# Kernel tuning notes

Measured on AMD Instinct MI355X. Metric: run time of the kernel, lower is better.

The kernel has to match this reference:

```python
import jax, jax.numpy as jnp
import numpy as np
import math

N = 4096      # n_history
D = 512       # embed_dim
H = 8         # time-weight MLP hidden size


def setup_inputs() -> dict:
    key = jax.random.key(0)
    k1, k2, k3, k4, k5 = jax.random.split(key, 5)
    return {
        "query_code_embeds": jax.random.normal(k1, (N, D), dtype=jnp.float32),
        "hist_embeddings": jax.random.normal(k2, (N, D), dtype=jnp.float32),
        "hist_times": jax.random.uniform(k3, (N,), dtype=jnp.float32),
        "tw_w1": jax.random.normal(k4, (1, H), dtype=jnp.float32) * (1.0 / math.sqrt(1.0)),
        "tw_b1": jnp.zeros((H,), dtype=jnp.float32),
        "tw_w2": jax.random.normal(k5, (H, 1), dtype=jnp.float32) * (1.0 / math.sqrt(H)),
        "tw_b2": jnp.zeros((1,), dtype=jnp.float32),
    }


def reference(query_code_embeds, hist_embeddings, hist_times, tw_w1, tw_b1, tw_w2, tw_b2):
    # pairwise absolute time differences: [n, n, 1]
    time_diffs = jnp.abs(hist_times[:, None] - hist_times[None, :])[..., None]
    # pointwise MLP on time diffs -> multiplicative attention bias [n, n]
    h = jax.nn.relu(time_diffs @ tw_w1 + tw_b1)            # [n, n, H]
    time_weights = jax.nn.sigmoid(h @ tw_w2 + tw_b2)[..., 0]  # [n, n]
    # scaled dot-product scores modulated by time weights
    scores = (query_code_embeds @ hist_embeddings.T) / math.sqrt(D)
    scores = scores * time_weights
    attn = jax.nn.softmax(scores, axis=1)
    return attn @ hist_embeddings
```

## Files before the change

kernel.cpp:

```cpp
#include <hip/hip_runtime.h>

#define N 4096
#define D 512
#define FRAG_SH 512
#define NTHR 256
#define SC_STRIDE 136
#define SMEM_BYTES 69632
#define BUF_SH 12288

typedef __attribute__((ext_vector_type(8))) short short8;
typedef __attribute__((ext_vector_type(4))) float f32x4;
typedef const __attribute__((address_space(1))) unsigned int* gptr_t;
typedef __attribute__((address_space(3))) unsigned int* lptr_t;

__device__ __forceinline__ unsigned short f2bf(float f) {
    unsigned int u = __float_as_uint(f);
    u = (u + 0x7FFFu + ((u >> 16) & 1u)) >> 16;
    return (unsigned short)u;
}
__device__ __forceinline__ unsigned short f2bf_rn(float f) {
    return (unsigned short)((__float_as_uint(f) + 0x8000u) >> 16);
}
__device__ __forceinline__ float bf2f(unsigned short u) {
    return __uint_as_float((unsigned)u << 16);
}

__global__ __launch_bounds__(NTHR) void prep_kernel(
    const float* __restrict__ q, const float* __restrict__ hist,
    unsigned short* __restrict__ Qblk, unsigned short* __restrict__ Kblk,
    unsigned short* __restrict__ Vblk, float* __restrict__ dsum)
{
    __shared__ unsigned short smem[32 * 512];
    const int bid = blockIdx.x, tid = threadIdx.x;
    if (bid >= 256) {
        int z = (bid - 256) * NTHR + tid;
        #pragma unroll
        for (int j = 0; j < 8; ++j) dsum[z * 8 + j] = 0.f;
        return;
    }
    const bool isQ = bid < 128;
    const int t = isQ ? bid : bid - 128;
    const float* src = isQ ? q : hist;
    const float scale = isQ ? 0.04419417382415922f : 1.0f;

    #pragma unroll
    for (int k = 0; k < 16; ++k) {
        int idx = tid + k * 256;
        int row = idx >> 7;
        int c4  = (idx & 127) << 2;
        float4 v = *(const float4*)(src + (size_t)(t * 32 + row) * D + c4);
        ushort4 o;
        o.x = f2bf(v.x * scale); o.y = f2bf(v.y * scale);
        o.z = f2bf(v.z * scale); o.w = f2bf(v.w * scale);
        *(ushort4*)(smem + row * 512 + c4) = o;
    }
    __syncthreads();

    unsigned short* ABdst = isQ ? Qblk : Kblk;
    #pragma unroll
    for (int k = 0; k < 8; ++k) {
        int s = tid + k * 256;
        int fl = s >> 6, ln = s & 63;
        int dk = fl >> 1, rbl = fl & 1;
        int l16 = ln & 15, qq = ln >> 4;
        short8 v = *(const short8*)(smem + (rbl * 16 + l16) * 512 + dk * 32 + qq * 8);
        *(short8*)(ABdst + ((size_t)dk * 256 + t * 2 + rbl) * FRAG_SH + ln * 8) = v;
    }
    if (!isQ) {
        #pragma unroll
        for (int k = 0; k < 8; ++k) {
            int s = tid + k * 256;
            int db = s >> 6, ln = s & 63;
            int l16 = ln & 15, qq = ln >> 4;
            unsigned short tmp[8];
            #pragma unroll
            for (int j = 0; j < 8; ++j)
                tmp[j] = smem[(qq * 8 + j) * 512 + db * 16 + l16];
            *(short8*)(Vblk + ((size_t)t * 32 + db) * FRAG_SH + ln * 8) = *(const short8*)tmp;
        }
    }
}

__global__ __launch_bounds__(NTHR, 2) void qk_kernel(
    const unsigned short* __restrict__ Qblk, const unsigned short* __restrict__ Kblk,
    const float* __restrict__ times,
    const float* __restrict__ w1, const float* __restrict__ b1,
    const float* __restrict__ w2, const float* __restrict__ b2,
    unsigned short* __restrict__ Pblk, float* __restrict__ dsum)
{
    extern __shared__ unsigned short smem[];
    const int tid = threadIdx.x, bid = blockIdx.x;
    const int wv = tid >> 6, lane = tid & 63;
    const int qq = lane >> 4, l16 = lane & 15;
    const int wy = wv >> 1, wx = wv & 1;
    const int cg = ((bid & 7) << 1) | ((bid >> 3) & 1);
    const int rg = bid >> 4;

    f32x4 acc[4][8];
    #pragma unroll
    for (int fy = 0; fy < 4; ++fy)
        #pragma unroll
        for (int fx = 0; fx < 8; ++fx) acc[fy][fx] = (f32x4){0.f, 0.f, 0.f, 0.f};

    auto stage = [&](int dk, int buf) {
        unsigned short* ldsb = smem + buf * BUF_SH;
        #pragma unroll
        for (int j = 0; j < 6; ++j) {
            const int s = wv * 6 + j;
            const unsigned short* g = (s < 8)
                ? (Qblk + ((size_t)dk * 256 + rg * 8 + s) * FRAG_SH + lane * 8)
                : (Kblk + ((size_t)dk * 256 + cg * 16 + (s - 8)) * FRAG_SH + lane * 8);
            __builtin_amdgcn_global_load_lds(
                (gptr_t)g, (lptr_t)(ldsb + s * FRAG_SH), 16, 0, 0);
        }
    };
    auto compute = [&](int buf) {
        const unsigned short* bufc = smem + buf * BUF_SH;
        short8 fa[4], fb[8];
        #pragma unroll
        for (int fy = 0; fy < 4; ++fy)
            fa[fy] = *(const short8*)(bufc + (wy * 4 + fy) * FRAG_SH + lane * 8);
        #pragma unroll
        for (int fx = 0; fx < 8; ++fx)
            fb[fx] = *(const short8*)(bufc + (8 + wx * 8 + fx) * FRAG_SH + lane * 8);
        #pragma unroll
        for (int fy = 0; fy < 4; ++fy)
            #pragma unroll
            for (int fx = 0; fx < 8; ++fx)
                acc[fy][fx] = __builtin_amdgcn_mfma_f32_16x16x32_bf16(fa[fy], fb[fx], acc[fy][fx], 0, 0, 0);
    };

    stage(0, 0);
    #pragma unroll 1
    for (int dk = 0; dk < 16; ++dk) {
        if (dk + 1 < 16) {
            stage(dk + 1, (dk + 1) & 1);
            asm volatile("s_waitcnt vmcnt(6)" ::: "memory");
        } else {
            asm volatile("s_waitcnt vmcnt(0)" ::: "memory");
        }
        __builtin_amdgcn_s_barrier();
        compute(dk & 1);
        __builtin_amdgcn_s_barrier();
    }

    float w1v[8], b1v[8], w2v[8];
    #pragma unroll
    for (int k = 0; k < 8; ++k) { w1v[k] = w1[k]; b1v[k] = b1[k]; w2v[k] = w2[k]; }
    const float b2v = b2[0];
    bool fast = true;
    #pragma unroll
    for (int k = 0; k < 8; ++k) fast = fast && (b1v[k] == 0.0f);
    float C1 = 0.0f;
    #pragma unroll
    for (int k = 0; k < 8; ++k) C1 += w2v[k] * fmaxf(w1v[k], 0.0f);

    const int rowbase = rg * 128 + wy * 64;
    const int colbase = cg * 256 + wx * 128;
    float tcol[8];
    #pragma unroll
    for (int fx = 0; fx < 8; ++fx) tcol[fx] = times[colbase + fx * 16 + l16];
    float trow[16];
    #pragma unroll
    for (int fy = 0; fy < 4; ++fy)
        #pragma unroll
        for (int ri = 0; ri < 4; ++ri)
            trow[fy * 4 + ri] = times[rowbase + fy * 16 + qq * 4 + ri];

    unsigned short* sc = smem + wv * (64 * SC_STRIDE);
    #pragma unroll
    for (int fy = 0; fy < 4; ++fy) {
        #pragma unroll
        for (int ri = 0; ri < 4; ++ri) {
            const float tq = trow[fy * 4 + ri];
            float se = 0.f;
            #pragma unroll
            for (int fx = 0; fx < 8; ++fx) {
                float td = fabsf(tq - tcol[fx]);
                float a = fmaf(td, C1, b2v);
                if (!fast) {
                    a = b2v;
                    #pragma unroll
                    for (int k = 0; k < 8; ++k)
                        a += w2v[k] * fmaxf(fmaf(td, w1v[k], b1v[k]), 0.f);
                }
                float twt = __builtin_amdgcn_rcpf(1.0f + __expf(-a));
                float e = __expf(acc[fy][fx][ri] * twt);
                se += e;
                sc[(fy * 16 + qq * 4 + ri) * SC_STRIDE + fx * 16 + l16] = f2bf_rn(e);
            }
            se += __shfl_xor(se, 1);
            se += __shfl_xor(se, 2);
            se += __shfl_xor(se, 4);
            se += __shfl_xor(se, 8);
            if (l16 == 0) atomicAdd(dsum + rowbase + fy * 16 + qq * 4 + ri, se);
        }
    }
    #pragma unroll
    for (int fy = 0; fy < 4; ++fy)
        #pragma unroll
        for (int kb2 = 0; kb2 < 4; ++kb2) {
            short8 v = *(const short8*)(sc + (fy * 16 + l16) * SC_STRIDE + kb2 * 32 + qq * 8);
            size_t fidx = (size_t)(cg * 8 + wx * 4 + kb2) * 256 + (rg * 8 + wy * 4 + fy);
            *(short8*)(Pblk + fidx * FRAG_SH + lane * 8) = v;
        }
}

template<int FY>
__global__ __launch_bounds__(NTHR, 2) void pv_kernel(
    const unsigned short* __restrict__ Pblk, const unsigned short* __restrict__ Vblk,
    unsigned short* __restrict__ Opart, int iters)
{
    const int tid = threadIdx.x;
    const int wv = tid >> 6, lane = tid & 63;
    const int qq = lane >> 4, l16 = lane & 15;
    const int chunk = blockIdx.x;
    const int rg = blockIdx.y;
    const int kbase = chunk * iters;

    f32x4 acc[FY][8];
    #pragma unroll
    for (int fy = 0; fy < FY; ++fy)
        #pragma unroll
        for (int fx = 0; fx < 8; ++fx) acc[fy][fx] = (f32x4){0.f, 0.f, 0.f, 0.f};

    for (int it = 0; it < iters; ++it) {
        const int kb32 = kbase + it;
        short8 a[FY], b[8];
        #pragma unroll
        for (int fy = 0; fy < FY; ++fy)
            a[fy] = *(const short8*)(Pblk + ((size_t)kb32 * 256 + rg * FY + fy) * FRAG_SH + lane * 8);
        #pragma unroll
        for (int fx = 0; fx < 8; ++fx)
            b[fx] = *(const short8*)(Vblk + ((size_t)kb32 * 32 + wv * 8 + fx) * FRAG_SH + lane * 8);
        __builtin_amdgcn_s_setprio(1);
        #pragma unroll
        for (int fy = 0; fy < FY; ++fy)
            #pragma unroll
            for (int fx = 0; fx < 8; ++fx)
                acc[fy][fx] = __builtin_amdgcn_mfma_f32_16x16x32_bf16(a[fy], b[fx], acc[fy][fx], 0, 0, 0);
        __builtin_amdgcn_s_setprio(0);
    }

    unsigned short* ob = Opart + (size_t)chunk * N * D;
    #pragma unroll
    for (int fy = 0; fy < FY; ++fy)
        #pragma unroll
        for (int ri = 0; ri < 4; ++ri) {
            const int row = rg * (FY * 16) + fy * 16 + qq * 4 + ri;
            #pragma unroll
            for (int fx = 0; fx < 8; ++fx) {
                const int col = wv * 128 + fx * 16 + l16;
                ob[(size_t)row * D + col] = f2bf_rn(acc[fy][fx][ri]);
            }
        }
}

__global__ __launch_bounds__(NTHR) void reduce_kernel(
    const unsigned short* __restrict__ Opart, const float* __restrict__ dsum,
    float* __restrict__ out, int KS2)
{
    int i = blockIdx.x * NTHR + threadIdx.x;
    int row = i >> 6;
    float inv = 1.0f / dsum[row];
    float acc[8] = {0.f, 0.f, 0.f, 0.f, 0.f, 0.f, 0.f, 0.f};
    for (int c = 0; c < KS2; ++c) {
        short8 u = ((const short8*)(Opart + (size_t)c * N * D))[i];
        #pragma unroll
        for (int j = 0; j < 8; ++j) acc[j] += bf2f((unsigned short)u[j]);
    }
    float4 o0 = {acc[0] * inv, acc[1] * inv, acc[2] * inv, acc[3] * inv};
    float4 o1 = {acc[4] * inv, acc[5] * inv, acc[6] * inv, acc[7] * inv};
    ((float4*)out)[i * 2 + 0] = o0;
    ((float4*)out)[i * 2 + 1] = o1;
}

extern "C" void kernel_launch(void* const* d_in, const int* in_sizes, int n_in,
                              void* d_out, int out_size, void* d_ws, size_t ws_size,
                              hipStream_t stream) {
    const float* q     = (const float*)d_in[0];
    const float* hist  = (const float*)d_in[1];
    const float* times = (const float*)d_in[2];
    const float* w1    = (const float*)d_in[3];
    const float* b1    = (const float*)d_in[4];
    const float* w2    = (const float*)d_in[5];
    const float* b2    = (const float*)d_in[6];
    float* out = (float*)d_out;

    char* base = (char*)d_ws;
    const size_t MB4 = (size_t)N * D * 2;
    unsigned short* Vblk = (unsigned short*)base;
    unsigned short* Pblk = (unsigned short*)(base + MB4);
    float* dsum          = (float*)(base + MB4 + (size_t)N * (size_t)N * 2);
    char* ob             = base + MB4 + (size_t)N * (size_t)N * 2 + 65536;
    unsigned short* Qblk = (unsigned short*)ob;
    unsigned short* Kblk = (unsigned short*)(ob + MB4);
    unsigned short* Opart = (unsigned short*)ob;
    const size_t fixed = (size_t)(ob - base);
    const int KS2 = (ws_size >= fixed + 8 * MB4) ? 8 :
                    (ws_size >= fixed + 4 * MB4) ? 4 : 2;
    const int iters = (N / 32) / KS2;

    (void)hipFuncSetAttribute((const void*)qk_kernel,
                        hipFuncAttributeMaxDynamicSharedMemorySize, SMEM_BYTES);

    prep_kernel<<<258, NTHR, 0, stream>>>(q, hist, Qblk, Kblk, Vblk, dsum);
    qk_kernel<<<512, NTHR, SMEM_BYTES, stream>>>(Qblk, Kblk, times, w1, b1, w2, b2, Pblk, dsum);
    if (KS2 == 8) {
        pv_kernel<4><<<dim3(KS2, N / 64), NTHR, 0, stream>>>(Pblk, Vblk, Opart, iters);
    } else {
        pv_kernel<2><<<dim3(KS2, N / 32), NTHR, 0, stream>>>(Pblk, Vblk, Opart, iters);
    }
    reduce_kernel<<<(N * D / 8) / NTHR, NTHR, 0, stream>>>(Opart, dsum, out, KS2);
}
```

Measured before the change: 132.6 us.

## Stage PV operand fragments through double-buffered LDS with async global-to-LDS loads

Adds a PV kernel that cooperatively prefetches the next iteration's P and V fragments into a double-buffered LDS region using global_load_lds. Each wave then reads its operands from LDS instead of issuing redundant global loads. The goal is to overlap memory latency with MFMA work and to stop every wave from re-fetching the shared P fragments. In exchange it adds two barriers per iteration and 72KB of LDS per block, which may limit occupancy to two blocks per CU. It also removes the s_setprio hints in the fallback kernel.

```diff
diff --git a/kernel.cpp b/kernel.cpp
--- a/kernel.cpp
+++ b/kernel.cpp
@@ -7,6 +7,8 @@
 #define SC_STRIDE 136
 #define SMEM_BYTES 69632
 #define BUF_SH 12288
+#define PV_BUF_SH 18432
+#define PV_SMEM_BYTES 73728
 
 typedef __attribute__((ext_vector_type(8))) short short8;
 typedef __attribute__((ext_vector_type(4))) float f32x4;
@@ -206,11 +208,11 @@
         }
 }
 
-template<int FY>
-__global__ __launch_bounds__(NTHR, 2) void pv_kernel(
+__global__ __launch_bounds__(NTHR, 2) void pv_staged_kernel(
     const unsigned short* __restrict__ Pblk, const unsigned short* __restrict__ Vblk,
     unsigned short* __restrict__ Opart, int iters)
 {
+    extern __shared__ unsigned short smem[];
     const int tid = threadIdx.x;
     const int wv = tid >> 6, lane = tid & 63;
     const int qq = lane >> 4, l16 = lane & 15;
@@ -218,6 +220,81 @@
     const int rg = blockIdx.y;
     const int kbase = chunk * iters;
 
+    f32x4 acc[4][8];
+    #pragma unroll
+    for (int fy = 0; fy < 4; ++fy)
+        #pragma unroll
+        for (int fx = 0; fx < 8; ++fx) acc[fy][fx] = (f32x4){0.f, 0.f, 0.f, 0.f};
+
+    auto stage = [&](int it, int buf) {
+        const int kb32 = kbase + it;
+        unsigned short* ldsb = smem + buf * PV_BUF_SH;
+        #pragma unroll
+        for (int j = 0; j < 9; ++j) {
+            const int s = wv * 9 + j;
+            const unsigned short* g = (s < 4)
+                ? (Pblk + ((size_t)kb32 * 256 + rg * 4 + s) * FRAG_SH + lane * 8)
+                : (Vblk + ((size_t)kb32 * 32 + (s - 4)) * FRAG_SH + lane * 8);
+            __builtin_amdgcn_global_load_lds(
+                (gptr_t)g, (lptr_t)(ldsb + s * FRAG_SH), 16, 0, 0);
+        }
+    };
+    auto compute = [&](int buf) {
+        const unsigned short* bufc = smem + buf * PV_BUF_SH;
+        short8 a[4], b[8];
+        #pragma unroll
+        for (int fy = 0; fy < 4; ++fy)
+            a[fy] = *(const short8*)(bufc + fy * FRAG_SH + lane * 8);
+        #pragma unroll
+        for (int fx = 0; fx < 8; ++fx)
+            b[fx] = *(const short8*)(bufc + (4 + wv * 8 + fx) * FRAG_SH + lane * 8);
+        #pragma unroll
+        for (int fy = 0; fy < 4; ++fy)
+            #pragma unroll
+            for (int fx = 0; fx < 8; ++fx)
+                acc[fy][fx] = __builtin_amdgcn_mfma_f32_16x16x32_bf16(a[fy], b[fx], acc[fy][fx], 0, 0, 0);
+    };
+
+    stage(0, 0);
+    #pragma unroll 1
+    for (int it = 0; it < iters; ++it) {
+        if (it + 1 < iters) {
+            stage(it + 1, (it + 1) & 1);
+            asm volatile("s_waitcnt vmcnt(9)" ::: "memory");
+        } else {
+            asm volatile("s_waitcnt vmcnt(0)" ::: "memory");
+        }
+        __builtin_amdgcn_s_barrier();
+        compute(it & 1);
+        __builtin_amdgcn_s_barrier();
+    }
+
+    unsigned short* ob = Opart + (size_t)chunk * N * D;
+    #pragma unroll
+    for (int fy = 0; fy < 4; ++fy)
+        #pragma unroll
+        for (int ri = 0; ri < 4; ++ri) {
+            const int row = rg * 64 + fy * 16 + qq * 4 + ri;
+            #pragma unroll
+            for (int fx = 0; fx < 8; ++fx) {
+                const int col = wv * 128 + fx * 16 + l16;
+                ob[(size_t)row * D + col] = f2bf_rn(acc[fy][fx][ri]);
+            }
+        }
+}
+
+template<int FY>
+__global__ __launch_bounds__(NTHR, 2) void pv_kernel(
+    const unsigned short* __restrict__ Pblk, const unsigned short* __restrict__ Vblk,
+    unsigned short* __restrict__ Opart, int iters)
+{
+    const int tid = threadIdx.x;
+    const int wv = tid >> 6, lane = tid & 63;
+    const int qq = lane >> 4, l16 = lane & 15;
+    const int chunk = blockIdx.x;
+    const int rg = blockIdx.y;
+    const int kbase = chunk * iters;
+
     f32x4 acc[FY][8];
     #pragma unroll
     for (int fy = 0; fy < FY; ++fy)
@@ -233,13 +310,11 @@
         #pragma unroll
         for (int fx = 0; fx < 8; ++fx)
             b[fx] = *(const short8*)(Vblk + ((size_t)kb32 * 32 + wv * 8 + fx) * FRAG_SH + lane * 8);
-        __builtin_amdgcn_s_setprio(1);
         #pragma unroll
         for (int fy = 0; fy < FY; ++fy)
             #pragma unroll
             for (int fx = 0; fx < 8; ++fx)
                 acc[fy][fx] = __builtin_amdgcn_mfma_f32_16x16x32_bf16(a[fy], b[fx], acc[fy][fx], 0, 0, 0);
-        __builtin_amdgcn_s_setprio(0);
     }
 
     unsigned short* ob = Opart + (size_t)chunk * N * D;
@@ -303,11 +378,13 @@
 
     (void)hipFuncSetAttribute((const void*)qk_kernel,
                         hipFuncAttributeMaxDynamicSharedMemorySize, SMEM_BYTES);
+    (void)hipFuncSetAttribute((const void*)pv_staged_kernel,
+                        hipFuncAttributeMaxDynamicSharedMemorySize, PV_SMEM_BYTES);
 
     prep_kernel<<<258, NTHR, 0, stream>>>(q, hist, Qblk, Kblk, Vblk, dsum);
     qk_kernel<<<512, NTHR, SMEM_BYTES, stream>>>(Qblk, Kblk, times, w1, b1, w2, b2, Pblk, dsum);
     if (KS2 == 8) {
-        pv_kernel<4><<<dim3(KS2, N / 64), NTHR, 0, stream>>>(Pblk, Vblk, Opart, iters);
+        pv_staged_kernel<<<dim3(KS2, N / 64), NTHR, PV_SMEM_BYTES, stream>>>(Pblk, Vblk, Opart, iters);
     } else {
         pv_kernel<2><<<dim3(KS2, N / 32), NTHR, 0, stream>>>(Pblk, Vblk, Opart, iters);
     }
```

Measured after the change: 134.9 us. Within noise of the previous version (+1.7%).

## Triple-buffer QK staging and replace split-K PV plus reduce with direct LDS-pipelined PV

Applied to the files above, without the earlier changes.

The QK kernel moves from double to triple buffering in shared memory, which lets it drop the trailing barrier in each k-step. The split-K PV kernel and the separate reduction kernel are replaced by a single PV kernel. That kernel stages P and V fragments into LDS with async global_load_lds double buffering, covers the full K range per block, and writes normalized fp32 output directly. This removes the bf16 partial-sum round trip and one launch. In exchange, each block does a long serial K loop with small 32x128 tiles, which reuses loaded data less.

```diff
diff --git a/kernel.cpp b/kernel.cpp
--- a/kernel.cpp
+++ b/kernel.cpp
@@ -5,8 +5,10 @@
 #define FRAG_SH 512
 #define NTHR 256
 #define SC_STRIDE 136
-#define SMEM_BYTES 69632
 #define BUF_SH 12288
+#define SMEM_BYTES 73728
+#define PVD_BUF_SH 10240
+#define PVD_SMEM_BYTES 40960
 
 typedef __attribute__((ext_vector_type(8))) short short8;
 typedef __attribute__((ext_vector_type(4))) float f32x4;
@@ -134,15 +136,15 @@
     #pragma unroll 1
     for (int dk = 0; dk < 16; ++dk) {
         if (dk + 1 < 16) {
-            stage(dk + 1, (dk + 1) & 1);
+            stage(dk + 1, (dk + 1) % 3);
             asm volatile("s_waitcnt vmcnt(6)" ::: "memory");
         } else {
             asm volatile("s_waitcnt vmcnt(0)" ::: "memory");
         }
         __builtin_amdgcn_s_barrier();
-        compute(dk & 1);
-        __builtin_amdgcn_s_barrier();
-    }
+        compute(dk % 3);
+    }
+    __builtin_amdgcn_s_barrier();
 
     float w1v[8], b1v[8], w2v[8];
     #pragma unroll
@@ -206,73 +208,88 @@
         }
 }
 
-template<int FY>
-__global__ __launch_bounds__(NTHR, 2) void pv_kernel(
+__global__ __launch_bounds__(NTHR, 2) void pv_direct_kernel(
     const unsigned short* __restrict__ Pblk, const unsigned short* __restrict__ Vblk,
-    unsigned short* __restrict__ Opart, int iters)
+    const float* __restrict__ dsum, float* __restrict__ out)
 {
+    extern __shared__ unsigned short smem[];
     const int tid = threadIdx.x;
     const int wv = tid >> 6, lane = tid & 63;
     const int qq = lane >> 4, l16 = lane & 15;
-    const int chunk = blockIdx.x;
+    const int cq = blockIdx.x;
     const int rg = blockIdx.y;
-    const int kbase = chunk * iters;
-
-    f32x4 acc[FY][8];
-    #pragma unroll
-    for (int fy = 0; fy < FY; ++fy)
-        #pragma unroll
-        for (int fx = 0; fx < 8; ++fx) acc[fy][fx] = (f32x4){0.f, 0.f, 0.f, 0.f};
-
-    for (int it = 0; it < iters; ++it) {
-        const int kb32 = kbase + it;
-        short8 a[FY], b[8];
-        #pragma unroll
-        for (int fy = 0; fy < FY; ++fy)
-            a[fy] = *(const short8*)(Pblk + ((size_t)kb32 * 256 + rg * FY + fy) * FRAG_SH + lane * 8);
-        #pragma unroll
-        for (int fx = 0; fx < 8; ++fx)
-            b[fx] = *(const short8*)(Vblk + ((size_t)kb32 * 32 + wv * 8 + fx) * FRAG_SH + lane * 8);
-        __builtin_amdgcn_s_setprio(1);
-        #pragma unroll
-        for (int fy = 0; fy < FY; ++fy)
-            #pragma unroll
-            for (int fx = 0; fx < 8; ++fx)
-                acc[fy][fx] = __builtin_amdgcn_mfma_f32_16x16x32_bf16(a[fy], b[fx], acc[fy][fx], 0, 0, 0);
-        __builtin_amdgcn_s_setprio(0);
-    }
-
-    unsigned short* ob = Opart + (size_t)chunk * N * D;
-    #pragma unroll
-    for (int fy = 0; fy < FY; ++fy)
+
+    f32x4 acc[2][2];
+    #pragma unroll
+    for (int fy = 0; fy < 2; ++fy)
+        #pragma unroll
+        for (int fx = 0; fx < 2; ++fx) acc[fy][fx] = (f32x4){0.f, 0.f, 0.f, 0.f};
+
+    auto stage = [&](int ph, int buf) {
+        unsigned short* ldsb = smem + buf * PVD_BUF_SH;
+        #pragma unroll
+        for (int j = 0; j < 5; ++j) {
+            const int s = wv * 5 + j;
+            const int u = s / 10, f = s % 10;
+            const int kb32 = ph * 2 + u;
+            const unsigned short* g = (f < 2)
+                ? (Pblk + ((size_t)kb32 * 256 + rg * 2 + f) * FRAG_SH + lane * 8)
+                : (Vblk + ((size_t)kb32 * 32 + cq * 8 + (f - 2)) * FRAG_SH + lane * 8);
+            __builtin_amdgcn_global_load_lds(
+                (gptr_t)g, (lptr_t)(ldsb + s * FRAG_SH), 16, 0, 0);
+        }
+    };
+    auto compute = [&](int buf) {
+        const unsigned short* bufc = smem + buf * PVD_BUF_SH;
+        #pragma unroll
+        for (int u = 0; u < 2; ++u) {
+            short8 a[2], b[2];
+            #pragma unroll
+            for (int fy = 0; fy < 2; ++fy)
+                a[fy] = *(const short8*)(bufc + (u * 10 + fy) * FRAG_SH + lane * 8);
+            #pragma unroll
+            for (int fx = 0; fx < 2; ++fx)
+                b[fx] = *(const short8*)(bufc + (u * 10 + 2 + wv * 2 + fx) * FRAG_SH + lane * 8);
+            #pragma unroll
+            for (int fy = 0; fy < 2; ++fy)
+                #pragma unroll
+                for (int fx = 0; fx < 2; ++fx)
+                    acc[fy][fx] = __builtin_amdgcn_mfma_f32_16x16x32_bf16(a[fy], b[fx], acc[fy][fx], 0, 0, 0);
+        }
+    };
+
+    stage(0, 0);
+    #pragma unroll 1
+    for (int ph = 0; ph < 64; ++ph) {
+        if (ph + 1 < 64) {
+            stage(ph + 1, (ph + 1) & 1);
+            asm volatile("s_waitcnt vmcnt(5)" ::: "memory");
+        } else {
+            asm volatile("s_waitcnt vmcnt(0)" ::: "memory");
+        }
+        __builtin_amdgcn_s_barrier();
+        compute(ph & 1);
+        __builtin_amdgcn_s_barrier();
+    }
+
+    float inv[2][4];
+    #pragma unroll
+    for (int fy = 0; fy < 2; ++fy)
+        #pragma unroll
+        for (int ri = 0; ri < 4; ++ri)
+            inv[fy][ri] = 1.0f / dsum[rg * 32 + fy * 16 + qq * 4 + ri];
+
+    #pragma unroll
+    for (int fy = 0; fy < 2; ++fy)
         #pragma unroll
         for (int ri = 0; ri < 4; ++ri) {
-            const int row = rg * (FY * 16) + fy * 16 + qq * 4 + ri;
-            #pragma unroll
-            for (int fx = 0; fx < 8; ++fx) {
-                const int col = wv * 128 + fx * 16 + l16;
-                ob[(size_t)row * D + col] = f2bf_rn(acc[fy][fx][ri]);
+            const int row = rg * 32 + fy * 16 + qq * 4 + ri;
+            #pragma unroll
+            for (int fx = 0; fx < 2; ++fx) {
+                const int col = cq * 128 + wv * 32 + fx * 16 + l16;
+                out[(size_t)row * D + col] = acc[fy][fx][ri] * inv[fy][ri];
             }
         }
-}
-
-__global__ __launch_bounds__(NTHR) void reduce_kernel(
-    const unsigned short* __restrict__ Opart, const float* __restrict__ dsum,
-    float* __restrict__ out, int KS2)
-{
-    int i = blockIdx.x * NTHR + threadIdx.x;
-    int row = i >> 6;
-    float inv = 1.0f / dsum[row];
-    float acc[8] = {0.f, 0.f, 0.f, 0.f, 0.f, 0.f, 0.f, 0.f};
-    for (int c = 0; c < KS2; ++c) {
-        short8 u = ((const short8*)(Opart + (size_t)c * N * D))[i];
-        #pragma unroll
-        for (int j = 0; j < 8; ++j) acc[j] += bf2f((unsigned short)u[j]);
-    }
-    float4 o0 = {acc[0] * inv, acc[1] * inv, acc[2] * inv, acc[3] * inv};
-    float4 o1 = {acc[4] * inv, acc[5] * inv, acc[6] * inv, acc[7] * inv};
-    ((float4*)out)[i * 2 + 0] = o0;
-    ((float4*)out)[i * 2 + 1] = o1;
 }
 
 extern "C" void kernel_launch(void* const* d_in, const int* in_sizes, int n_in,
@@ -295,21 +312,13 @@
     char* ob             = base + MB4 + (size_t)N * (size_t)N * 2 + 65536;
     unsigned short* Qblk = (unsigned short*)ob;
     unsigned short* Kblk = (unsigned short*)(ob + MB4);
-    unsigned short* Opart = (unsigned short*)ob;
-    const size_t fixed = (size_t)(ob - base);
-    const int KS2 = (ws_size >= fixed + 8 * MB4) ? 8 :
-                    (ws_size >= fixed + 4 * MB4) ? 4 : 2;
-    const int iters = (N / 32) / KS2;
 
     (void)hipFuncSetAttribute((const void*)qk_kernel,
                         hipFuncAttributeMaxDynamicSharedMemorySize, SMEM_BYTES);
+    (void)hipFuncSetAttribute((const void*)pv_direct_kernel,
+                        hipFuncAttributeMaxDynamicSharedMemorySize, PVD_SMEM_BYTES);
 
     prep_kernel<<<258, NTHR, 0, stream>>>(q, hist, Qblk, Kblk, Vblk, dsum);
     qk_kernel<<<512, NTHR, SMEM_BYTES, stream>>>(Qblk, Kblk, times, w1, b1, w2, b2, Pblk, dsum);
-    if (KS2 == 8) {
-        pv_kernel<4><<<dim3(KS2, N / 64), NTHR, 0, stream>>>(Pblk, Vblk, Opart, iters);
-    } else {
-        pv_kernel<2><<<dim3(KS2, N / 32), NTHR, 0, stream>>>(Pblk, Vblk, Opart, iters);
-    }
-    reduce_kernel<<<(N * D / 8) / NTHR, NTHR, 0, stream>>>(Opart, dsum, out, KS2);
-}
+    pv_direct_kernel<<<dim3(4, N / 32), NTHR, PVD_SMEM_BYTES, stream>>>(Pblk, Vblk, dsum, out);
+}
```

New measurement: 137.2 us. 3.5% more time.
